# Optimization experiments

Measured on AMD Instinct MI355X. Metric: run time of the kernel, lower is better.

The kernel has to match this reference:

```python
import jax, jax.numpy as jnp
from jax import lax
import numpy as np

IMG = 1024                      # image_size (square)
RPN_TRAIN_THRES = 0.5
RATIOS = jnp.array([0.5, 1.0, 2.0], jnp.float32)
SCALES = jnp.array([0.2, 0.4, 0.7], jnp.float32)
K_GT = 16


def _conv(x, w, b, stride):
    # NHWC x HWIO -> NHWC, VALID padding (keras Conv2D default)
    return lax.conv_general_dilated(x, w, (stride, stride), 'VALID',
                                    dimension_numbers=('NHWC', 'HWIO', 'NHWC')) + b


def _anchor_set():
    # [-w/2, -h/2, w/2, h/2] for 9 ratio/scale combos
    rs = jnp.sqrt(RATIOS)[:, None]                      # (3,1)
    ws = (SCALES[None, :] * rs).reshape(-1)             # (9,)
    hs = (SCALES[None, :] / rs).reshape(-1)
    return jnp.stack([ws, hs, ws, hs], axis=1) * 0.5 * jnp.array([-1.0, -1.0, 1.0, 1.0], jnp.float32)


def _anchors_pre(h, w):
    # mirrors generate_anchors_pre (incl. tf.transpose reversing axes -> (W,H,4));
    # feature map is square here so the layout matches the original.
    x = jnp.arange(0.0, 1.0, 1.0 / w, dtype=jnp.float32)
    y = jnp.arange(0.0, 1.0, 1.0 / h, dtype=jnp.float32)
    xx, yy = jnp.meshgrid(x, y)                         # (H,W)
    centers = jnp.stack([xx, yy, xx, yy], 0).transpose(2, 1, 0)  # (W,H,4)
    return centers[:, :, None, :] + _anchor_set()       # (W,H,9,4)


def _iou(b1, b2, gw, gh):
    gwh = jnp.array([gw, gh], jnp.float32)
    s1 = jnp.prod(b1[..., 2:] - b1[..., :2] + gwh, axis=-1)
    s2 = jnp.prod(b2[..., 2:] - b2[..., :2] + gwh, axis=-1)
    xa = jnp.maximum(b1[..., 0], b2[..., 0])
    ya = jnp.maximum(b1[..., 1], b2[..., 1])
    xb = jnp.minimum(b1[..., 2], b2[..., 2])
    yb = jnp.minimum(b1[..., 3], b2[..., 3])
    inter = jnp.maximum(xb - xa + gw, 0.0) * jnp.maximum(yb - ya + gh, 0.0)
    return inter / (s1 + s2 - inter)


def setup_inputs() -> dict:
    key = jax.random.key(0)
    ks = jax.random.split(key, 10)
    image = jax.random.uniform(ks[0], (1, IMG, IMG, 3), jnp.float32)
    cxy = jax.random.uniform(ks[1], (K_GT, 2), jnp.float32, 0.2, 0.8)
    wh = jax.random.uniform(ks[2], (K_GT, 2), jnp.float32, 0.1, 0.4)
    gt_boxes = jnp.concatenate([cxy - wh / 2, cxy + wh / 2], axis=1)  # (K,4) x1,y1,x2,y2
    Wb = jax.random.normal(ks[3], (4, 4, 3, 128), jnp.float32) * 0.05
    bb = jnp.zeros((128,), jnp.float32)
    Wi = jax.random.normal(ks[4], (3, 3, 128, 256), jnp.float32) * 0.05
    bi = jnp.zeros((256,), jnp.float32)
    Wc = jax.random.normal(ks[5], (1, 1, 256, 9), jnp.float32) * 0.05
    bc = jnp.zeros((9,), jnp.float32)
    Wr = jax.random.normal(ks[6], (1, 1, 256, 36), jnp.float32) * 0.05
    br = jnp.zeros((36,), jnp.float32)
    return {'image': image, 'gt_boxes': gt_boxes, 'Wb': Wb, 'bb': bb,
            'Wi': Wi, 'bi': bi, 'Wc': Wc, 'bc': bc, 'Wr': Wr, 'br': br}


def reference(image, gt_boxes, Wb, bb, Wi, bi, Wc, bc, Wr, br):
    feats = _conv(image, Wb, bb, 4)            # backbone: (1,256,256,128)
    fmap = _conv(feats, Wi, bi, 1)             # inter_conv: (1,254,254,256)
    fh, fw = fmap.shape[1], fmap.shape[2]
    gw = 1.0 / IMG
    gh = 1.0 / IMG
    anchors = _anchors_pre(fh, fw).reshape(-1, 4)          # (N,4), N = fh*fw*9
    inside = ((anchors[:, 0] >= 0.0) & (anchors[:, 1] >= 0.0) &
              (anchors[:, 2] < 1.0) & (anchors[:, 3] < 1.0))
    iou = _iou(anchors[:, None, :], gt_boxes[None, :, :], gw, gh)  # (N,K)
    max_iou = jnp.max(iou, axis=1)
    iou_in = jnp.where(inside[:, None], iou, -1.0)
    gt_max_iou = jnp.max(iou_in, axis=0)                   # (K,)
    is_gt_best = jnp.any((iou_in == gt_max_iou[None, :]) & inside[:, None], axis=1)
    pos = inside & (is_gt_best | (max_iou >= RPN_TRAIN_THRES))
    labels = jnp.where(inside, 0.0, -1.0)
    labels = jnp.where(pos, 1.0, labels)                   # (N,) in {-1,0,1}
    # RPN classification loss (BCE with logits) over labels != -1
    cls = _conv(fmap, Wc, bc, 1).reshape(-1)               # (N,)
    sel = (labels != -1.0).astype(jnp.float32)
    lbl = jnp.maximum(labels, 0.0)
    bce = lbl * jax.nn.softplus(-cls) + (1.0 - lbl) * jax.nn.softplus(cls)
    cls_loss = jnp.sum(bce * sel) / jnp.sum(sel)
    # smooth-L1 box loss, faithful to the original (it masks bbox_pred, not the diff)
    reg = _conv(fmap, Wr, br, 1).reshape(-1, 4)            # (N,4)
    m = pos.astype(jnp.float32)[:, None]                   # (N,1) bbox_mask
    ab = jnp.abs(reg * m)
    ss = (ab < 1.0).astype(jnp.float32)
    box_loss = ab * ab * 0.5 * ss + (ab - 0.5) * (1.0 - ss)
    bbox_loss = jnp.sum(box_loss) / jnp.sum(m)
    return cls_loss + bbox_loss
```

## Files before the change

### kernel.cpp

```cpp
#include <hip/hip_runtime.h>

#define F2      254
#define NPIX    (F2 * F2)
#define KGT     16
#define GWC     (1.0f / 1024.0f)

typedef __attribute__((ext_vector_type(8))) short bf16x8;
typedef __attribute__((ext_vector_type(4))) float f32x4;

__device__ unsigned short g_feats[256 * 256 * 128];
__device__ unsigned short g_W2s[36 * 3 * 64 * 8];
__device__ float          g_b2[48];
__device__ float          g_acc[4] = {0.0f, 0.0f, 0.0f, 0.0f};
__device__ unsigned       g_keys[KGT] = {
    0x407FFFFFu, 0x407FFFFFu, 0x407FFFFFu, 0x407FFFFFu,
    0x407FFFFFu, 0x407FFFFFu, 0x407FFFFFu, 0x407FFFFFu,
    0x407FFFFFu, 0x407FFFFFu, 0x407FFFFFu, 0x407FFFFFu,
    0x407FFFFFu, 0x407FFFFFu, 0x407FFFFFu, 0x407FFFFFu};
__device__ unsigned       g_done = 0u;

__device__ __forceinline__ float b2f(unsigned short h) {
    return __uint_as_float(((unsigned)h) << 16);
}
__device__ __forceinline__ unsigned short f2b(float f) {
    unsigned u = __float_as_uint(f);
    unsigned r = (u + 0x7FFFu + ((u >> 16) & 1u)) >> 16;
    return (unsigned short)r;
}

__device__ __forceinline__ void iou16(float x1, float y1, float x2, float y2,
                                      const float* __restrict__ gt, float* __restrict__ v) {
    float s1 = (x2 - x1 + GWC) * (y2 - y1 + GWC);
#pragma unroll
    for (int k = 0; k < KGT; ++k) {
        float gx1 = gt[k * 4 + 0], gy1 = gt[k * 4 + 1];
        float gx2 = gt[k * 4 + 2], gy2 = gt[k * 4 + 3];
        float s2 = (gx2 - gx1 + GWC) * (gy2 - gy1 + GWC);
        float xa = fmaxf(x1, gx1), ya = fmaxf(y1, gy1);
        float xb = fminf(x2, gx2), yb = fminf(y2, gy2);
        float iw = fmaxf(xb - xa + GWC, 0.0f);
        float ih = fmaxf(yb - ya + GWC, 0.0f);
        float inter = iw * ih;
        v[k] = inter / (s1 + s2 - inter);
    }
}

__device__ __forceinline__ void type_extent(int a, float* hw, float* hh) {
    int ri = a / 3, si = a - ri * 3;
    float rat = (ri == 0) ? 0.5f : (ri == 1) ? 1.0f : 2.0f;
    float scl = (si == 0) ? 0.2f : (si == 1) ? 0.4f : 0.7f;
    float rs = sqrtf(rat);
    *hw = scl * rs * 0.5f;
    *hh = scl / rs * 0.5f;
}

__device__ __forceinline__ bf16x8 ld_a8(const float* ib, int kbase) {
    int r0 = kbase / 12, q0 = kbase - r0 * 12;
    unsigned short a8[8];
    float4 f0 = *(const float4*)(ib + (size_t)r0 * 3072 + q0);
    int k4 = kbase + 4;
    int r1 = k4 / 12, q1 = k4 - r1 * 12;
    float4 f1 = *(const float4*)(ib + (size_t)r1 * 3072 + q1);
    a8[0] = f2b(f0.x); a8[1] = f2b(f0.y); a8[2] = f2b(f0.z); a8[3] = f2b(f0.w);
    a8[4] = f2b(f1.x); a8[5] = f2b(f1.y); a8[6] = f2b(f1.z); a8[7] = f2b(f1.w);
    return *(bf16x8*)a8;
}

__global__ __launch_bounds__(256) void k_front(const float* __restrict__ img,
                                               const float* __restrict__ bb,
                                               const float* __restrict__ Wb,
                                               const float* __restrict__ Wi,
                                               const float* __restrict__ bi,
                                               const float* __restrict__ Wc,
                                               const float* __restrict__ bc,
                                               const float* __restrict__ Wr,
                                               const float* __restrict__ br,
                                               const float* __restrict__ gt) {
    __shared__ alignas(16) char sbuf[128 * 48 * 4];
    __shared__ float red[4][KGT];
    int t = threadIdx.x;
    int b = blockIdx.x;

    if (b < 1024) {
        unsigned short* wbs = (unsigned short*)sbuf;
#pragma unroll
        for (int it = 0; it < 4; ++it) {
            int e = t + it * 256;
            int kt = e >> 9, nt = (e >> 6) & 7, l = e & 63;
            unsigned short w8[8];
#pragma unroll
            for (int j = 0; j < 8; ++j) {
                int k = kt * 32 + ((l >> 4) * 8) + j;
                int oc = nt * 16 + (l & 15);
                w8[j] = (k < 48) ? f2b(Wb[(size_t)k * 128 + oc]) : (unsigned short)0;
            }
            *(ulonglong2*)(wbs + (size_t)e * 8) = *(ulonglong2*)w8;
        }
        __syncthreads();

        int cid = ((b & 7) << 7) + (b >> 3);
        int l = t & 63;
        int quad = l >> 4;
        int tile = cid * 4 + (t >> 6);
        int m0 = tile * 16;
        int p = m0 + (l & 15);
        int oy = p >> 8, ox = p & 255;
        const float* ib = img + ((size_t)oy * 4 * 1024 + (size_t)ox * 4) * 3;

        bf16x8 a0 = ld_a8(ib, quad * 8);
        bf16x8 a1 = (quad < 2) ? ld_a8(ib, 32 + quad * 8) : (bf16x8){0, 0, 0, 0, 0, 0, 0, 0};

        f32x4 acc[8];
#pragma unroll
        for (int nt = 0; nt < 8; ++nt) acc[nt] = (f32x4){0.0f, 0.0f, 0.0f, 0.0f};
#pragma unroll
        for (int nt = 0; nt < 8; ++nt) {
            bf16x8 b0 = *(const bf16x8*)(wbs + (size_t)(nt * 64 + l) * 8);
            bf16x8 b1 = *(const bf16x8*)(wbs + (size_t)((8 + nt) * 64 + l) * 8);
            acc[nt] = __builtin_amdgcn_mfma_f32_16x16x32_bf16(a0, b0, acc[nt], 0, 0, 0);
            acc[nt] = __builtin_amdgcn_mfma_f32_16x16x32_bf16(a1, b1, acc[nt], 0, 0, 0);
        }

        int n0 = l & 15;
        int mB = m0 + quad * 4;
#pragma unroll
        for (int nt = 0; nt < 8; ++nt) {
            int oc = nt * 16 + n0;
            float bias = bb[oc];
#pragma unroll
            for (int r = 0; r < 4; ++r) {
                g_feats[(size_t)(mB + r) * 128 + oc] = f2b(acc[nt][r] + bias);
            }
        }
        return;
    }

    if (b < 1312) {
        float (*wcr2)[48] = (float (*)[48])sbuf;
        int bw = b - 1024;
        int wave = __builtin_amdgcn_readfirstlane(t >> 6);
        int lane = t & 63;
        int k = bw * 4 + wave;
        int o = min(lane, 47);
        const float* wik = Wi + (size_t)k * 256;
        float acc = 0.0f;
        bool bias_thr = (b == 1024) && (t < 48);
        float a2 = 0.0f;
        if (bias_thr) a2 = (t < 9) ? bc[t] : ((t < 45) ? br[t - 9] : 0.0f);

        for (int pss = 0; pss < 2; ++pss) {
            __syncthreads();
            int ocb = pss * 128;
            for (int i = t; i < 1152; i += 256) {
                int oc = i / 9;
                wcr2[oc][i % 9] = Wc[(size_t)(ocb + oc) * 9 + i % 9];
            }
            for (int i = t; i < 4608; i += 256) {
                int oc = i / 36;
                wcr2[oc][9 + i % 36] = Wr[(size_t)(ocb + oc) * 36 + i % 36];
            }
            for (int i = t; i < 384; i += 256) wcr2[i / 3][45 + i % 3] = 0.0f;
            __syncthreads();
#pragma unroll 8
            for (int oc = 0; oc < 128; ++oc)
                acc = fmaf(wik[ocb + oc], wcr2[oc][o], acc);
            if (bias_thr) {
                for (int oc = 0; oc < 128; ++oc)
                    a2 = fmaf(bi[ocb + oc], wcr2[oc][t], a2);
            }
        }

        if (lane < 48) {
            int kt = k >> 5, r5 = k & 31, j = r5 & 7, lhi = r5 >> 3;
            int nt = o >> 4, llo = o & 15, l2 = lhi * 16 + llo;
            g_W2s[(size_t)((kt * 3 + nt) * 64 + l2) * 8 + j] = f2b(acc);
        }
        if (bias_thr) g_b2[t] = a2;
        return;
    }

    {
        int bid = b - 1312;
        int a = bid >> 5;
        int blk = bid & 31;
        float hw, hh;
        type_extent(a, &hw, &hh);
        float m16[KGT];
#pragma unroll
        for (int k = 0; k < KGT; ++k) m16[k] = -1.0f;
        for (int pix = blk * 256 + t; pix < NPIX; pix += 32 * 256) {
            int w = pix / F2, h = pix - w * F2;
            float cx = (float)w * (1.0f / 254.0f);
            float cy = (float)h * (1.0f / 254.0f);
            float x1 = cx - hw, y1 = cy - hh, x2 = cx + hw, y2 = cy + hh;
            bool inside = (x1 >= 0.0f) && (y1 >= 0.0f) && (x2 < 1.0f) && (y2 < 1.0f);
            if (__ballot(inside) == 0ull) continue;
            if (inside) {
                float v[KGT];
                iou16(x1, y1, x2, y2, gt, v);
#pragma unroll
                for (int k = 0; k < KGT; ++k) m16[k] = fmaxf(m16[k], v[k]);
            }
        }
#pragma unroll
        for (int k = 0; k < KGT; ++k) {
#pragma unroll
            for (int m = 32; m; m >>= 1) m16[k] = fmaxf(m16[k], __shfl_xor(m16[k], m, 64));
        }
        int lane = t & 63, wv = t >> 6;
        if (lane == 0) {
#pragma unroll
            for (int k = 0; k < KGT; ++k) red[wv][k] = m16[k];
        }
        __syncthreads();
        if (t < KGT) {
            float mx = fmaxf(fmaxf(red[0][t], red[1][t]), fmaxf(red[2][t], red[3][t]));
            unsigned u = __float_as_uint(mx);
            unsigned key = (u & 0x80000000u) ? ~u : (u | 0x80000000u);
            atomicMax(&g_keys[t], key);
        }
    }
}

__global__ __launch_bounds__(256) void k_convC_loss(const float* __restrict__ gt,
                                                    unsigned* __restrict__ out) {
    __shared__ alignas(16) unsigned short Bs[12 * 1536];
    __shared__ float redl[4][4];
    int t = threadIdx.x;
    int b = blockIdx.x;
    int xcd = b & 7;
    int cid = (xcd == 0) ? (b >> 3) : (64 + (xcd - 1) * 63 + (b >> 3));
    int l = t & 63;
    int quad = l >> 4;
    int wv = t >> 6;
    int tile = cid * 4 + wv;
    int m0 = tile * 32;
    int mA0 = min(m0 + (l & 15), NPIX - 1);
    int mA1 = min(m0 + 16 + (l & 15), NPIX - 1);
    int py0 = mA0 / F2, px0 = mA0 - py0 * F2;
    int py1 = mA1 / F2, px1 = mA1 - py1 * F2;

    f32x4 acc[2][3];
#pragma unroll
    for (int h = 0; h < 2; ++h)
#pragma unroll
        for (int nt = 0; nt < 3; ++nt) acc[h][nt] = (f32x4){0.0f, 0.0f, 0.0f, 0.0f};

    for (int c = 0; c < 3; ++c) {
        __syncthreads();
        {
            const uint4* src = (const uint4*)(g_W2s + (size_t)c * 18432);
            uint4* dst = (uint4*)Bs;
#pragma unroll
            for (int j = 0; j < 9; ++j) dst[t + 256 * j] = src[t + 256 * j];
        }
        __syncthreads();
#pragma unroll
        for (int i = 0; i < 12; ++i) {
            int kt = c * 12 + i;
            int pos = kt >> 2, kc = kt & 3;
            int ky = pos / 3, kx = pos - ky * 3;
            const unsigned short* ap0 =
                g_feats + ((size_t)(py0 + ky) * 256 + (px0 + kx)) * 128 + quad * 8 + kc * 32;
            const unsigned short* ap1 =
                g_feats + ((size_t)(py1 + ky) * 256 + (px1 + kx)) * 128 + quad * 8 + kc * 32;
            bf16x8 a0 = *(const bf16x8*)ap0;
            bf16x8 a1 = *(const bf16x8*)ap1;
            const unsigned short* bp = Bs + (size_t)i * 1536 + l * 8;
            bf16x8 b0 = *(const bf16x8*)(bp);
            bf16x8 b1 = *(const bf16x8*)(bp + 512);
            bf16x8 b2v = *(const bf16x8*)(bp + 1024);
            acc[0][0] = __builtin_amdgcn_mfma_f32_16x16x32_bf16(a0, b0, acc[0][0], 0, 0, 0);
            acc[0][1] = __builtin_amdgcn_mfma_f32_16x16x32_bf16(a0, b1, acc[0][1], 0, 0, 0);
            acc[0][2] = __builtin_amdgcn_mfma_f32_16x16x32_bf16(a0, b2v, acc[0][2], 0, 0, 0);
            acc[1][0] = __builtin_amdgcn_mfma_f32_16x16x32_bf16(a1, b0, acc[1][0], 0, 0, 0);
            acc[1][1] = __builtin_amdgcn_mfma_f32_16x16x32_bf16(a1, b1, acc[1][1], 0, 0, 0);
            acc[1][2] = __builtin_amdgcn_mfma_f32_16x16x32_bf16(a1, b2v, acc[1][2], 0, 0, 0);
        }
    }

    __syncthreads();
    float (*S)[129] = (float (*)[129])(void*)Bs;
    int n0 = l & 15;
#pragma unroll
    for (int h = 0; h < 2; ++h) {
        int plB = wv * 32 + h * 16 + quad * 4;
#pragma unroll
        for (int nt = 0; nt < 3; ++nt) {
            int n = nt * 16 + n0;
            float bias = g_b2[n];
#pragma unroll
            for (int r = 0; r < 4; ++r) S[n][plB + r] = acc[h][nt][r] + bias;
        }
    }
    __syncthreads();

    int m0b = cid * 128;
    float sb = 0.0f, ss = 0.0f, sx = 0.0f, sp = 0.0f;
    for (int idx = t; idx < 1152; idx += 256) {
        int a = idx >> 7;
        int pl = idx & 127;
        int m = m0b + pl;
        float hw, hhf;
        type_extent(a, &hw, &hhf);
        bool inside = false;
        float x1 = 0.0f, y1 = 0.0f, x2 = 0.0f, y2 = 0.0f;
        if (m < NPIX) {
            int pw = m / F2, ph = m - pw * F2;
            float cx = (float)pw * (1.0f / 254.0f);
            float cy = (float)ph * (1.0f / 254.0f);
            x1 = cx - hw; y1 = cy - hhf; x2 = cx + hw; y2 = cy + hhf;
            inside = (x1 >= 0.0f) && (y1 >= 0.0f) && (x2 < 1.0f) && (y2 < 1.0f);
        }
        if (__ballot(inside) == 0ull) continue;
        if (inside) {
            float v[KGT];
            iou16(x1, y1, x2, y2, gt, v);
            float maxi = -1.0f;
            bool best = false;
#pragma unroll
            for (int k = 0; k < KGT; ++k) {
                maxi = fmaxf(maxi, v[k]);
                unsigned e = g_keys[k];
                float gm = __uint_as_float((e & 0x80000000u) ? (e & 0x7FFFFFFFu) : ~e);
                best = best || (v[k] == gm);
            }
            bool ispos = best || (maxi >= 0.5f);
            float c = b2f(f2b(S[a][pl]));
            float z = ispos ? -c : c;
            sb += fmaxf(z, 0.0f) + log1pf(expf(-fabsf(z)));
            ss += 1.0f;
            if (ispos) {
                float aa;
                aa = fabsf(b2f(f2b(S[9 + 4 * a + 0][pl]))); sx += (aa < 1.0f) ? 0.5f * aa * aa : aa - 0.5f;
                aa = fabsf(b2f(f2b(S[9 + 4 * a + 1][pl]))); sx += (aa < 1.0f) ? 0.5f * aa * aa : aa - 0.5f;
                aa = fabsf(b2f(f2b(S[9 + 4 * a + 2][pl]))); sx += (aa < 1.0f) ? 0.5f * aa * aa : aa - 0.5f;
                aa = fabsf(b2f(f2b(S[9 + 4 * a + 3][pl]))); sx += (aa < 1.0f) ? 0.5f * aa * aa : aa - 0.5f;
                sp += 1.0f;
            }
        }
    }

#pragma unroll
    for (int mm = 32; mm; mm >>= 1) {
        sb += __shfl_xor(sb, mm, 64);
        ss += __shfl_xor(ss, mm, 64);
        sx += __shfl_xor(sx, mm, 64);
        sp += __shfl_xor(sp, mm, 64);
    }
    int lane = t & 63;
    if (lane == 0) { redl[wv][0] = sb; redl[wv][1] = ss; redl[wv][2] = sx; redl[wv][3] = sp; }
    __syncthreads();
    if (t < 4) {
        float s = redl[0][t] + redl[1][t] + redl[2][t] + redl[3][t];
        atomicAdd(&g_acc[t], s);
    }
    __syncthreads();
    if (t == 0) {
        unsigned prev = atomicAdd(&g_done, 1u);
        if (prev == 504u) {
            float a0 = atomicAdd(&g_acc[0], 0.0f);
            float a1 = atomicAdd(&g_acc[1], 0.0f);
            float a2 = atomicAdd(&g_acc[2], 0.0f);
            float a3 = atomicAdd(&g_acc[3], 0.0f);
            float res = a0 / a1 + a2 / a3;
            unsigned lo = (unsigned)f2b(res);
            unsigned hi = __float_as_uint(res) >> 16;
            out[0] = (hi << 16) | lo;
            g_acc[0] = 0.0f; g_acc[1] = 0.0f; g_acc[2] = 0.0f; g_acc[3] = 0.0f;
#pragma unroll
            for (int k = 0; k < KGT; ++k) g_keys[k] = 0x407FFFFFu;
            g_done = 0u;
        }
    }
}

extern "C" void kernel_launch(void* const* d_in, const int* in_sizes, int n_in,
                              void* d_out, int out_size, void* d_ws, size_t ws_size,
                              hipStream_t stream) {
    (void)in_sizes; (void)n_in; (void)out_size; (void)d_ws; (void)ws_size;
    const float* image = (const float*)d_in[0];
    const float* gt    = (const float*)d_in[1];
    const float* Wb    = (const float*)d_in[2];
    const float* bb    = (const float*)d_in[3];
    const float* Wi    = (const float*)d_in[4];
    const float* bi    = (const float*)d_in[5];
    const float* Wc    = (const float*)d_in[6];
    const float* bc    = (const float*)d_in[7];
    const float* Wr    = (const float*)d_in[8];
    const float* br    = (const float*)d_in[9];

    k_front     <<<1600, 256, 0, stream>>>(image, bb, Wb, Wi, bi, Wc, bc, Wr, br, gt);
    k_convC_loss<<<505, 256, 0, stream>>>(gt, (unsigned*)d_out);
}
```

Baseline: 125.7 us.

## Fuse front and conv-loss kernels into one persistent kernel with grid barrier

Merges the two launches into a single 512-block kernel. Each block does two backbone conv tiles, then either the weight-folding work or the anchor-IoU max work, then waits on a global atomic barrier before running the conv/loss stage. This removes a kernel launch boundary and the tail of the first kernel. The cost is a spin-wait grid barrier that depends on all 512 blocks being co-resident (launch_bounds 256,2), and reduced parallelism for the IoU scan (24 blocks per anchor instead of 32).

```diff
diff --git a/kernel.cpp b/kernel.cpp
--- a/kernel.cpp
+++ b/kernel.cpp
@@ -18,6 +18,7 @@
     0x407FFFFFu, 0x407FFFFFu, 0x407FFFFFu, 0x407FFFFFu,
     0x407FFFFFu, 0x407FFFFFu, 0x407FFFFFu, 0x407FFFFFu};
 __device__ unsigned       g_done = 0u;
+__device__ unsigned       g_bar  = 0u;
 
 __device__ __forceinline__ float b2f(unsigned short h) {
     return __uint_as_float(((unsigned)h) << 16);
@@ -66,22 +67,23 @@
     return *(bf16x8*)a8;
 }
 
-__global__ __launch_bounds__(256) void k_front(const float* __restrict__ img,
-                                               const float* __restrict__ bb,
-                                               const float* __restrict__ Wb,
-                                               const float* __restrict__ Wi,
-                                               const float* __restrict__ bi,
-                                               const float* __restrict__ Wc,
-                                               const float* __restrict__ bc,
-                                               const float* __restrict__ Wr,
-                                               const float* __restrict__ br,
-                                               const float* __restrict__ gt) {
-    __shared__ alignas(16) char sbuf[128 * 48 * 4];
+__global__ __launch_bounds__(256, 2) void k_all(const float* __restrict__ img,
+                                                const float* __restrict__ bb,
+                                                const float* __restrict__ Wb,
+                                                const float* __restrict__ Wi,
+                                                const float* __restrict__ bi,
+                                                const float* __restrict__ Wc,
+                                                const float* __restrict__ bc,
+                                                const float* __restrict__ Wr,
+                                                const float* __restrict__ br,
+                                                const float* __restrict__ gt,
+                                                unsigned* __restrict__ out) {
+    __shared__ alignas(16) char sbuf[36864];
     __shared__ float red[4][KGT];
     int t = threadIdx.x;
     int b = blockIdx.x;
 
-    if (b < 1024) {
+    {
         unsigned short* wbs = (unsigned short*)sbuf;
 #pragma unroll
         for (int it = 0; it < 4; ++it) {
@@ -98,53 +100,53 @@
         }
         __syncthreads();
 
-        int cid = ((b & 7) << 7) + (b >> 3);
         int l = t & 63;
         int quad = l >> 4;
-        int tile = cid * 4 + (t >> 6);
-        int m0 = tile * 16;
-        int p = m0 + (l & 15);
-        int oy = p >> 8, ox = p & 255;
-        const float* ib = img + ((size_t)oy * 4 * 1024 + (size_t)ox * 4) * 3;
-
-        bf16x8 a0 = ld_a8(ib, quad * 8);
-        bf16x8 a1 = (quad < 2) ? ld_a8(ib, 32 + quad * 8) : (bf16x8){0, 0, 0, 0, 0, 0, 0, 0};
-
-        f32x4 acc[8];
-#pragma unroll
-        for (int nt = 0; nt < 8; ++nt) acc[nt] = (f32x4){0.0f, 0.0f, 0.0f, 0.0f};
-#pragma unroll
-        for (int nt = 0; nt < 8; ++nt) {
-            bf16x8 b0 = *(const bf16x8*)(wbs + (size_t)(nt * 64 + l) * 8);
-            bf16x8 b1 = *(const bf16x8*)(wbs + (size_t)((8 + nt) * 64 + l) * 8);
-            acc[nt] = __builtin_amdgcn_mfma_f32_16x16x32_bf16(a0, b0, acc[nt], 0, 0, 0);
-            acc[nt] = __builtin_amdgcn_mfma_f32_16x16x32_bf16(a1, b1, acc[nt], 0, 0, 0);
-        }
-
-        int n0 = l & 15;
-        int mB = m0 + quad * 4;
-#pragma unroll
-        for (int nt = 0; nt < 8; ++nt) {
-            int oc = nt * 16 + n0;
-            float bias = bb[oc];
-#pragma unroll
-            for (int r = 0; r < 4; ++r) {
-                g_feats[(size_t)(mB + r) * 128 + oc] = f2b(acc[nt][r] + bias);
-            }
-        }
-        return;
-    }
-
-    if (b < 1312) {
+        for (int half = 0; half < 2; ++half) {
+            int cid = ((b & 7) << 7) + half * 64 + (b >> 3);
+            int tile = cid * 4 + (t >> 6);
+            int m0 = tile * 16;
+            int p = m0 + (l & 15);
+            int oy = p >> 8, ox = p & 255;
+            const float* ib = img + ((size_t)oy * 4 * 1024 + (size_t)ox * 4) * 3;
+
+            bf16x8 a0 = ld_a8(ib, quad * 8);
+            bf16x8 a1 = (quad < 2) ? ld_a8(ib, 32 + quad * 8) : (bf16x8){0, 0, 0, 0, 0, 0, 0, 0};
+
+            f32x4 acc[8];
+#pragma unroll
+            for (int nt = 0; nt < 8; ++nt) acc[nt] = (f32x4){0.0f, 0.0f, 0.0f, 0.0f};
+#pragma unroll
+            for (int nt = 0; nt < 8; ++nt) {
+                bf16x8 b0 = *(const bf16x8*)(wbs + (size_t)(nt * 64 + l) * 8);
+                bf16x8 b1 = *(const bf16x8*)(wbs + (size_t)((8 + nt) * 64 + l) * 8);
+                acc[nt] = __builtin_amdgcn_mfma_f32_16x16x32_bf16(a0, b0, acc[nt], 0, 0, 0);
+                acc[nt] = __builtin_amdgcn_mfma_f32_16x16x32_bf16(a1, b1, acc[nt], 0, 0, 0);
+            }
+
+            int n0 = l & 15;
+            int mB = m0 + quad * 4;
+#pragma unroll
+            for (int nt = 0; nt < 8; ++nt) {
+                int oc = nt * 16 + n0;
+                float bias = bb[oc];
+#pragma unroll
+                for (int r = 0; r < 4; ++r) {
+                    g_feats[(size_t)(mB + r) * 128 + oc] = f2b(acc[nt][r] + bias);
+                }
+            }
+        }
+    }
+
+    if (b < 288) {
         float (*wcr2)[48] = (float (*)[48])sbuf;
-        int bw = b - 1024;
         int wave = __builtin_amdgcn_readfirstlane(t >> 6);
         int lane = t & 63;
-        int k = bw * 4 + wave;
+        int k = b * 4 + wave;
         int o = min(lane, 47);
         const float* wik = Wi + (size_t)k * 256;
         float acc = 0.0f;
-        bool bias_thr = (b == 1024) && (t < 48);
+        bool bias_thr = (b == 0) && (t < 48);
         float a2 = 0.0f;
         if (bias_thr) a2 = (t < 9) ? bc[t] : ((t < 45) ? br[t - 9] : 0.0f);
 
@@ -176,19 +178,18 @@
             g_W2s[(size_t)((kt * 3 + nt) * 64 + l2) * 8 + j] = f2b(acc);
         }
         if (bias_thr) g_b2[t] = a2;
-        return;
-    }
-
-    {
-        int bid = b - 1312;
-        int a = bid >> 5;
-        int blk = bid & 31;
+    }
+
+    if (b >= 288 && b < 504) {
+        int unit = b - 288;
+        int a = unit / 24;
+        int blk = unit % 24;
         float hw, hh;
         type_extent(a, &hw, &hh);
         float m16[KGT];
 #pragma unroll
         for (int k = 0; k < KGT; ++k) m16[k] = -1.0f;
-        for (int pix = blk * 256 + t; pix < NPIX; pix += 32 * 256) {
+        for (int pix = blk * 256 + t; pix < NPIX; pix += 24 * 256) {
             int w = pix / F2, h = pix - w * F2;
             float cx = (float)w * (1.0f / 254.0f);
             float cy = (float)h * (1.0f / 254.0f);
@@ -208,6 +209,7 @@
             for (int m = 32; m; m >>= 1) m16[k] = fmaxf(m16[k], __shfl_xor(m16[k], m, 64));
         }
         int lane = t & 63, wv = t >> 6;
+        __syncthreads();
         if (lane == 0) {
 #pragma unroll
             for (int k = 0; k < KGT; ++k) red[wv][k] = m16[k];
@@ -220,14 +222,22 @@
             atomicMax(&g_keys[t], key);
         }
     }
-}
-
-__global__ __launch_bounds__(256) void k_convC_loss(const float* __restrict__ gt,
-                                                    unsigned* __restrict__ out) {
-    __shared__ alignas(16) unsigned short Bs[12 * 1536];
-    __shared__ float redl[4][4];
-    int t = threadIdx.x;
-    int b = blockIdx.x;
+
+    __syncthreads();
+    __threadfence();
+    if (t == 0) {
+        unsigned prev = __hip_atomic_fetch_add(&g_bar, 1u, __ATOMIC_ACQ_REL,
+                                               __HIP_MEMORY_SCOPE_AGENT);
+        unsigned target = ((prev >> 9) + 1u) << 9;
+        while (__hip_atomic_load(&g_bar, __ATOMIC_ACQUIRE, __HIP_MEMORY_SCOPE_AGENT) < target)
+            __builtin_amdgcn_s_sleep(2);
+    }
+    __syncthreads();
+    __threadfence();
+
+    if (b >= 505) return;
+
+    unsigned short* Bs = (unsigned short*)sbuf;
     int xcd = b & 7;
     int cid = (xcd == 0) ? (b >> 3) : (64 + (xcd - 1) * 63 + (b >> 3));
     int l = t & 63;
@@ -280,7 +290,7 @@
     }
 
     __syncthreads();
-    float (*S)[129] = (float (*)[129])(void*)Bs;
+    float (*S)[129] = (float (*)[129])(void*)sbuf;
     int n0 = l & 15;
 #pragma unroll
     for (int h = 0; h < 2; ++h) {
@@ -349,10 +359,10 @@
         sp += __shfl_xor(sp, mm, 64);
     }
     int lane = t & 63;
-    if (lane == 0) { redl[wv][0] = sb; redl[wv][1] = ss; redl[wv][2] = sx; redl[wv][3] = sp; }
+    if (lane == 0) { red[wv][0] = sb; red[wv][1] = ss; red[wv][2] = sx; red[wv][3] = sp; }
     __syncthreads();
     if (t < 4) {
-        float s = redl[0][t] + redl[1][t] + redl[2][t] + redl[3][t];
+        float s = red[0][t] + red[1][t] + red[2][t] + red[3][t];
         atomicAdd(&g_acc[t], s);
     }
     __syncthreads();
@@ -390,6 +400,6 @@
     const float* Wr    = (const float*)d_in[8];
     const float* br    = (const float*)d_in[9];
 
-    k_front     <<<1600, 256, 0, stream>>>(image, bb, Wb, Wi, bi, Wc, bc, Wr, br, gt);
-    k_convC_loss<<<505, 256, 0, stream>>>(gt, (unsigned*)d_out);
-}
+    k_all<<<512, 256, 0, stream>>>(image, bb, Wb, Wi, bi, Wc, bc, Wr, br, gt,
+                                   (unsigned*)d_out);
+}
```

New measurement: 255.0 us. 103% more time.
